# Optimization experiments

Hardware: AMD Instinct MI355X
Metric: run time of the kernel (lower is better)

The kernel has to match this reference:

```python
import jax, jax.numpy as jnp
import numpy as np

N_AGENTS = 64
B = 256
D = 256  # hidden_size == comm_dim


def setup_inputs() -> dict:
    key = jax.random.key(0)
    ks = jax.random.split(key, 4)
    s = 1.0 / np.sqrt(D)
    return {
        "hidden_state": jax.random.normal(ks[0], (B * N_AGENTS, D), jnp.float32),
        "W_act": jax.random.normal(ks[1], (D, D), jnp.float32) * s,
        "b_act": jnp.zeros((D,), jnp.float32),
        "W_sum": jax.random.normal(ks[2], (D, D), jnp.float32) * s,
        "b_sum": jnp.zeros((D,), jnp.float32),
        "W_head": jax.random.normal(ks[3], (D, D), jnp.float32) * s,
        "b_head": jnp.zeros((D,), jnp.float32),
    }


def reference(hidden_state, W_act, b_act, W_sum, b_sum, W_head, b_head):
    n = N_AGENTS
    # comm_act linear: (b*n, D)
    comm = hidden_state @ W_act.T + b_act
    b = comm.shape[0] // n
    comm = comm.reshape(b, n, D)
    # comm_mask = ones(n,n) - eye(n); agents all alive, comm_action_one=True
    mask = (jnp.ones((n, n), comm.dtype) - jnp.eye(n, dtype=comm.dtype))
    # original: expand to (b,n,n,D), mask, divide by (n-1), sum over dim=1 (sender i)
    # fused equivalent: out[b,j,d] = sum_i mask[i,j] * comm[b,i,d] / (n-1)
    agg = jnp.einsum('ij,bid->bjd', mask, comm) / (n - 1)
    x = agg.reshape(b * n, D) @ W_sum.T + b_sum      # comm_sum_head
    out = jax.nn.relu(x @ W_head.T + b_head)          # comm_head + active_fun
    return out
```

## Files before the change

### kernel.cpp

```cpp
#include <hip/hip_runtime.h>
#include <hip/hip_bf16.h>

#define DIM 256
#define NAGENT 64
#define NBATCH 256

typedef __bf16 bf16_t;
typedef bf16_t bf16x4 __attribute__((ext_vector_type(4)));
typedef bf16_t bf16x8 __attribute__((ext_vector_type(8)));
typedef float f32x4 __attribute__((ext_vector_type(4)));

__global__ __launch_bounds__(1024) void prep_kernel(
    const float* __restrict__ Wh, const float* __restrict__ Ws,
    const float* __restrict__ Wa, const float* __restrict__ ba,
    const float* __restrict__ bs, const float* __restrict__ bh,
    bf16_t* __restrict__ Wc, float* __restrict__ bcw) {
  const int b = blockIdx.x;
  const int t = threadIdx.x;
  const int jg = t & 63;
  const int kc = t >> 6;

  __shared__ float whl[DIM];
  __shared__ float t1l[DIM];
  __shared__ f32x4 part[16][64];
  __shared__ float red[256];

  if (t < DIM) whl[t] = Wh[b * DIM + t];
  __syncthreads();

  {
    f32x4 a = {0.f, 0.f, 0.f, 0.f};
#pragma unroll
    for (int ki = 0; ki < 16; ++ki) {
      const int k = kc * 16 + ki;
      const f32x4 w4 = *(const f32x4*)&Ws[k * DIM + jg * 4];
      a += whl[k] * w4;
    }
    part[kc][jg] = a;
  }
  __syncthreads();
  if (t < 64) {
    f32x4 s = part[0][t];
#pragma unroll
    for (int kc2 = 1; kc2 < 16; ++kc2) s += part[kc2][t];
    *(f32x4*)&t1l[t * 4] = s;
  }
  __syncthreads();

  {
    f32x4 a = {0.f, 0.f, 0.f, 0.f};
#pragma unroll
    for (int ki = 0; ki < 16; ++ki) {
      const int k = kc * 16 + ki;
      const f32x4 w4 = *(const f32x4*)&Wa[k * DIM + jg * 4];
      a += t1l[k] * w4;
    }
    if (t < 256) red[t] = t1l[t] * ba[t] + whl[t] * bs[t];
    part[kc][jg] = a;
  }
  __syncthreads();
  if (t < 64) {
    f32x4 s = part[0][t];
#pragma unroll
    for (int kc2 = 1; kc2 < 16; ++kc2) s += part[kc2][t];
    bf16x4 wb;
    wb[0] = (bf16_t)s[0]; wb[1] = (bf16_t)s[1];
    wb[2] = (bf16_t)s[2]; wb[3] = (bf16_t)s[3];
    *(bf16x4*)&Wc[b * DIM + t * 4] = wb;
    float p = red[t] + red[t + 64] + red[t + 128] + red[t + 192];
#pragma unroll
    for (int s2 = 32; s2 > 0; s2 >>= 1) p += __shfl_down(p, s2, 64);
    if (t == 0) bcw[b] = p + bh[b];
  }
}

__global__ __launch_bounds__(512) void fused_kernel(
    const float* __restrict__ h, const bf16_t* __restrict__ Wc,
    const float* __restrict__ bcw, float* __restrict__ out) {
  const int b = blockIdx.x;
  const int t = threadIdx.x;

  __shared__ __align__(16) bf16_t g[NAGENT * DIM];
  __shared__ f32x4 ps[8][64];

  const float* hb = h + (size_t)b * NAGENT * DIM;
  const int cg = t & 63;
  const int rg = t >> 6;

  f32x4 v[8];
  f32x4 s4 = {0.f, 0.f, 0.f, 0.f};
#pragma unroll
  for (int i = 0; i < 8; ++i) {
    v[i] = *(const f32x4*)&hb[(rg * 8 + i) * DIM + cg * 4];
    s4 += v[i];
  }
  ps[rg][cg] = s4;
  __syncthreads();
  f32x4 hs = ps[0][cg];
#pragma unroll
  for (int r = 1; r < 8; ++r) hs += ps[r][cg];

  const float inv = 1.0f / 63.0f;
#pragma unroll
  for (int i = 0; i < 8; ++i) {
    const int row = rg * 8 + i;
    const f32x4 gv = (hs - v[i]) * inv;
    bf16x4 gb;
    gb[0] = (bf16_t)gv[0]; gb[1] = (bf16_t)gv[1];
    gb[2] = (bf16_t)gv[2]; gb[3] = (bf16_t)gv[3];
    *(bf16x4*)&g[row * DIM + ((cg * 4) ^ ((row & 7) << 3))] = gb;
  }
  __syncthreads();

  const int w = t >> 6, lane = t & 63;
  const int lrow = lane & 15, lgrp = lane >> 4;

  f32x4 acc[4][2];
#pragma unroll
  for (int rt = 0; rt < 4; ++rt)
#pragma unroll
    for (int ct = 0; ct < 2; ++ct) acc[rt][ct] = (f32x4){0.f, 0.f, 0.f, 0.f};

#pragma unroll
  for (int kk = 0; kk < 8; ++kk) {
    const int k0 = kk * 32 + lgrp * 8;
    bf16x8 bfrag[2];
#pragma unroll
    for (int ct = 0; ct < 2; ++ct) {
      const int col = w * 32 + ct * 16 + lrow;
      bfrag[ct] = *(const bf16x8*)&Wc[col * DIM + k0];
    }
#pragma unroll
    for (int rt = 0; rt < 4; ++rt) {
      const int arow = rt * 16 + lrow;
      const bf16x8 afrag =
          *(const bf16x8*)&g[arow * DIM + (k0 ^ ((arow & 7) << 3))];
      acc[rt][0] = __builtin_amdgcn_mfma_f32_16x16x32_bf16(afrag, bfrag[0], acc[rt][0], 0, 0, 0);
      acc[rt][1] = __builtin_amdgcn_mfma_f32_16x16x32_bf16(afrag, bfrag[1], acc[rt][1], 0, 0, 0);
    }
  }

  float* ob = out + (size_t)b * NAGENT * DIM;
#pragma unroll
  for (int ct = 0; ct < 2; ++ct) {
    const int col = w * 32 + ct * 16 + lrow;
    const float bcv = bcw[col];
#pragma unroll
    for (int rt = 0; rt < 4; ++rt) {
#pragma unroll
      for (int r = 0; r < 4; ++r) {
        const int row = rt * 16 + lgrp * 4 + r;
        const float val = acc[rt][ct][r] + bcv;
        ob[row * DIM + col] = val > 0.f ? val : 0.f;
      }
    }
  }
}

extern "C" void kernel_launch(void* const* d_in, const int* in_sizes, int n_in,
                              void* d_out, int out_size, void* d_ws, size_t ws_size,
                              hipStream_t stream) {
  const float* h  = (const float*)d_in[0];
  const float* Wa = (const float*)d_in[1];
  const float* ba = (const float*)d_in[2];
  const float* Ws = (const float*)d_in[3];
  const float* bs = (const float*)d_in[4];
  const float* Wh = (const float*)d_in[5];
  const float* bh = (const float*)d_in[6];
  float* out = (float*)d_out;

  char* ws = (char*)d_ws;
  bf16_t* Wc  = (bf16_t*)ws;
  float*  bcw = (float*)(ws + 128 * 1024);

  prep_kernel<<<NBATCH, 1024, 0, stream>>>(Wh, Ws, Wa, ba, bs, bh, Wc, bcw);
  fused_kernel<<<NBATCH, 512, 0, stream>>>(h, Wc, bcw, out);
}
```

Baseline: 23.65 us.

## Fuse weight-prep and main kernels via grid-wide atomic readiness barrier

Merges the weight-composition prep kernel into the main fused kernel. Each block computes one row of the combined weight and bias, publishes it, and increments a global ready counter. It then overlaps the hidden-state load and aggregation with that work and spin-waits until all 256 blocks have finished before starting the MFMA GEMM. This removes a kernel launch and the inter-kernel gap, but adds a memset, a spin barrier that relies on all 256 blocks being co-resident, and 512-thread prep work in place of 1024 threads.

Result: slower. 67.83 us (+186.7%).

```diff
diff --git a/kernel.cpp b/kernel.cpp
--- a/kernel.cpp
+++ b/kernel.cpp
@@ -10,39 +10,45 @@
 typedef bf16_t bf16x8 __attribute__((ext_vector_type(8)));
 typedef float f32x4 __attribute__((ext_vector_type(4)));
 
-__global__ __launch_bounds__(1024) void prep_kernel(
+__global__ __launch_bounds__(512) void mac_one_kernel(
+    const float* __restrict__ h,
     const float* __restrict__ Wh, const float* __restrict__ Ws,
     const float* __restrict__ Wa, const float* __restrict__ ba,
     const float* __restrict__ bs, const float* __restrict__ bh,
-    bf16_t* __restrict__ Wc, float* __restrict__ bcw) {
+    bf16_t* __restrict__ Wc, float* __restrict__ bcw,
+    unsigned int* ready, float* __restrict__ out) {
   const int b = blockIdx.x;
   const int t = threadIdx.x;
-  const int jg = t & 63;
-  const int kc = t >> 6;
+  const int cg = t & 63;
+  const int rg = t >> 6;
 
-  __shared__ float whl[DIM];
+  __shared__ __align__(16) bf16_t g[NAGENT * DIM];
+  __shared__ f32x4 ps[8][64];
+  __shared__ f32x4 part[8][64];
   __shared__ float t1l[DIM];
-  __shared__ f32x4 part[16][64];
-  __shared__ float red[256];
 
-  if (t < DIM) whl[t] = Wh[b * DIM + t];
-  __syncthreads();
+  const float* hb = h + (size_t)b * NAGENT * DIM;
+
+  f32x4 v[8];
+#pragma unroll
+  for (int i = 0; i < 8; ++i)
+    v[i] = *(const f32x4*)&hb[(rg * 8 + i) * DIM + cg * 4];
 
   {
     f32x4 a = {0.f, 0.f, 0.f, 0.f};
 #pragma unroll
-    for (int ki = 0; ki < 16; ++ki) {
-      const int k = kc * 16 + ki;
-      const f32x4 w4 = *(const f32x4*)&Ws[k * DIM + jg * 4];
-      a += whl[k] * w4;
+    for (int ki = 0; ki < 32; ++ki) {
+      const int k = rg * 32 + ki;
+      const float wv = Wh[b * DIM + k];
+      a += wv * *(const f32x4*)&Ws[k * DIM + cg * 4];
     }
-    part[kc][jg] = a;
+    part[rg][cg] = a;
   }
   __syncthreads();
   if (t < 64) {
     f32x4 s = part[0][t];
 #pragma unroll
-    for (int kc2 = 1; kc2 < 16; ++kc2) s += part[kc2][t];
+    for (int r = 1; r < 8; ++r) s += part[r][t];
     *(f32x4*)&t1l[t * 4] = s;
   }
   __syncthreads();
@@ -50,56 +56,44 @@
   {
     f32x4 a = {0.f, 0.f, 0.f, 0.f};
 #pragma unroll
-    for (int ki = 0; ki < 16; ++ki) {
-      const int k = kc * 16 + ki;
-      const f32x4 w4 = *(const f32x4*)&Wa[k * DIM + jg * 4];
-      a += t1l[k] * w4;
+    for (int ki = 0; ki < 32; ++ki) {
+      const int k = rg * 32 + ki;
+      a += t1l[k] * *(const f32x4*)&Wa[k * DIM + cg * 4];
     }
-    if (t < 256) red[t] = t1l[t] * ba[t] + whl[t] * bs[t];
-    part[kc][jg] = a;
+    f32x4 s4 = v[0];
+#pragma unroll
+    for (int i = 1; i < 8; ++i) s4 += v[i];
+    ps[rg][cg] = s4;
+    part[rg][cg] = a;
   }
   __syncthreads();
+
   if (t < 64) {
     f32x4 s = part[0][t];
 #pragma unroll
-    for (int kc2 = 1; kc2 < 16; ++kc2) s += part[kc2][t];
+    for (int r = 1; r < 8; ++r) s += part[r][t];
     bf16x4 wb;
     wb[0] = (bf16_t)s[0]; wb[1] = (bf16_t)s[1];
     wb[2] = (bf16_t)s[2]; wb[3] = (bf16_t)s[3];
     *(bf16x4*)&Wc[b * DIM + t * 4] = wb;
-    float p = red[t] + red[t + 64] + red[t + 128] + red[t + 192];
+    const f32x4 t14 = *(const f32x4*)&t1l[t * 4];
+    const f32x4 ba4 = *(const f32x4*)&ba[t * 4];
+    const f32x4 wh4 = *(const f32x4*)&Wh[b * DIM + t * 4];
+    const f32x4 bs4 = *(const f32x4*)&bs[t * 4];
+    const f32x4 pp = t14 * ba4 + wh4 * bs4;
+    float p = pp[0] + pp[1] + pp[2] + pp[3];
 #pragma unroll
     for (int s2 = 32; s2 > 0; s2 >>= 1) p += __shfl_down(p, s2, 64);
-    if (t == 0) bcw[b] = p + bh[b];
+    if (t == 0) {
+      bcw[b] = p + bh[b];
+      __threadfence();
+      atomicAdd(ready, 1u);
+    }
   }
-}
 
-__global__ __launch_bounds__(512) void fused_kernel(
-    const float* __restrict__ h, const bf16_t* __restrict__ Wc,
-    const float* __restrict__ bcw, float* __restrict__ out) {
-  const int b = blockIdx.x;
-  const int t = threadIdx.x;
-
-  __shared__ __align__(16) bf16_t g[NAGENT * DIM];
-  __shared__ f32x4 ps[8][64];
-
-  const float* hb = h + (size_t)b * NAGENT * DIM;
-  const int cg = t & 63;
-  const int rg = t >> 6;
-
-  f32x4 v[8];
-  f32x4 s4 = {0.f, 0.f, 0.f, 0.f};
-#pragma unroll
-  for (int i = 0; i < 8; ++i) {
-    v[i] = *(const f32x4*)&hb[(rg * 8 + i) * DIM + cg * 4];
-    s4 += v[i];
-  }
-  ps[rg][cg] = s4;
-  __syncthreads();
   f32x4 hs = ps[0][cg];
 #pragma unroll
   for (int r = 1; r < 8; ++r) hs += ps[r][cg];
-
   const float inv = 1.0f / 63.0f;
 #pragma unroll
   for (int i = 0; i < 8; ++i) {
@@ -112,7 +106,15 @@
   }
   __syncthreads();
 
-  const int w = t >> 6, lane = t & 63;
+  if (t == 0) {
+    while (__hip_atomic_load(ready, __ATOMIC_ACQUIRE,
+                             __HIP_MEMORY_SCOPE_AGENT) < NBATCH)
+      __builtin_amdgcn_s_sleep(4);
+  }
+  __syncthreads();
+  __threadfence();
+
+  const int w = rg, lane = t & 63;
   const int lrow = lane & 15, lgrp = lane >> 4;
 
   f32x4 acc[4][2];
@@ -172,7 +174,10 @@
   char* ws = (char*)d_ws;
   bf16_t* Wc  = (bf16_t*)ws;
   float*  bcw = (float*)(ws + 128 * 1024);
+  unsigned int* ready = (unsigned int*)(ws + 132 * 1024);
 
-  prep_kernel<<<NBATCH, 1024, 0, stream>>>(Wh, Ws, Wa, ba, bs, bh, Wc, bcw);
-  fused_kernel<<<NBATCH, 512, 0, stream>>>(h, Wc, bcw, out);
+  hipMemsetAsync(ready, 0, sizeof(unsigned int), stream);
+
+  mac_one_kernel<<<NBATCH, 512, 0, stream>>>(h, Wh, Ws, Wa, ba, bs, bh,
+                                             Wc, bcw, ready, out);
 }
```

## Replace weight-product precompute with three chained in-block MFMA GEMMs

Applied to the files above, without the earlier changes.

Removes the prep kernel that folded W_head·W_sum·W_act into one combined bf16 weight and bias. The single fused kernel now runs three successive MFMA GEMM stages per batch block, ping-ponging bf16 activations between two shared-memory buffers and converting fp32 weights to bf16 on the fly. This saves a kernel launch and the serial prep work, but triples the MFMA work and weight traffic per block, doubles LDS use, and rounds intermediates to bf16 more often.

Measured after the change: 35.28 us. 49.2% more time.

```diff
diff --git a/kernel.cpp b/kernel.cpp
--- a/kernel.cpp
+++ b/kernel.cpp
@@ -10,82 +10,84 @@
 typedef bf16_t bf16x8 __attribute__((ext_vector_type(8)));
 typedef float f32x4 __attribute__((ext_vector_type(4)));
 
-__global__ __launch_bounds__(1024) void prep_kernel(
-    const float* __restrict__ Wh, const float* __restrict__ Ws,
-    const float* __restrict__ Wa, const float* __restrict__ ba,
-    const float* __restrict__ bs, const float* __restrict__ bh,
-    bf16_t* __restrict__ Wc, float* __restrict__ bcw) {
-  const int b = blockIdx.x;
-  const int t = threadIdx.x;
-  const int jg = t & 63;
-  const int kc = t >> 6;
+template <bool FINAL>
+__device__ __forceinline__ void gemm_stage(
+    const bf16_t* gin, const float* __restrict__ W,
+    const float* __restrict__ bias, bf16_t* gout,
+    float* __restrict__ gmem_out, int w, int lane) {
+  const int lrow = lane & 15, lgrp = lane >> 4;
 
-  __shared__ float whl[DIM];
-  __shared__ float t1l[DIM];
-  __shared__ f32x4 part[16][64];
-  __shared__ float red[256];
+  f32x4 acc[4][2];
+#pragma unroll
+  for (int rt = 0; rt < 4; ++rt)
+#pragma unroll
+    for (int ct = 0; ct < 2; ++ct) acc[rt][ct] = (f32x4){0.f, 0.f, 0.f, 0.f};
 
-  if (t < DIM) whl[t] = Wh[b * DIM + t];
-  __syncthreads();
+  float bv[2];
+#pragma unroll
+  for (int ct = 0; ct < 2; ++ct) bv[ct] = bias[w * 32 + ct * 16 + lrow];
 
-  {
-    f32x4 a = {0.f, 0.f, 0.f, 0.f};
 #pragma unroll
-    for (int ki = 0; ki < 16; ++ki) {
-      const int k = kc * 16 + ki;
-      const f32x4 w4 = *(const f32x4*)&Ws[k * DIM + jg * 4];
-      a += whl[k] * w4;
+  for (int kk = 0; kk < 8; ++kk) {
+    const int k0 = kk * 32 + lgrp * 8;
+    bf16x8 bfrag[2];
+#pragma unroll
+    for (int ct = 0; ct < 2; ++ct) {
+      const int col = w * 32 + ct * 16 + lrow;
+      const f32x4 w0 = *(const f32x4*)&W[col * DIM + k0];
+      const f32x4 w1 = *(const f32x4*)&W[col * DIM + k0 + 4];
+      bf16x8 bf;
+      bf[0] = (bf16_t)w0[0]; bf[1] = (bf16_t)w0[1];
+      bf[2] = (bf16_t)w0[2]; bf[3] = (bf16_t)w0[3];
+      bf[4] = (bf16_t)w1[0]; bf[5] = (bf16_t)w1[1];
+      bf[6] = (bf16_t)w1[2]; bf[7] = (bf16_t)w1[3];
+      bfrag[ct] = bf;
     }
-    part[kc][jg] = a;
+#pragma unroll
+    for (int rt = 0; rt < 4; ++rt) {
+      const int arow = rt * 16 + lrow;
+      const bf16x8 afrag =
+          *(const bf16x8*)&gin[arow * DIM + (k0 ^ ((arow & 7) << 3))];
+      acc[rt][0] = __builtin_amdgcn_mfma_f32_16x16x32_bf16(afrag, bfrag[0], acc[rt][0], 0, 0, 0);
+      acc[rt][1] = __builtin_amdgcn_mfma_f32_16x16x32_bf16(afrag, bfrag[1], acc[rt][1], 0, 0, 0);
+    }
   }
-  __syncthreads();
-  if (t < 64) {
-    f32x4 s = part[0][t];
+
 #pragma unroll
-    for (int kc2 = 1; kc2 < 16; ++kc2) s += part[kc2][t];
-    *(f32x4*)&t1l[t * 4] = s;
-  }
-  __syncthreads();
-
-  {
-    f32x4 a = {0.f, 0.f, 0.f, 0.f};
+  for (int ct = 0; ct < 2; ++ct) {
+    const int col = w * 32 + ct * 16 + lrow;
 #pragma unroll
-    for (int ki = 0; ki < 16; ++ki) {
-      const int k = kc * 16 + ki;
-      const f32x4 w4 = *(const f32x4*)&Wa[k * DIM + jg * 4];
-      a += t1l[k] * w4;
+    for (int rt = 0; rt < 4; ++rt) {
+#pragma unroll
+      for (int r = 0; r < 4; ++r) {
+        const int row = rt * 16 + lgrp * 4 + r;
+        float val = acc[rt][ct][r] + bv[ct];
+        if (FINAL) {
+          gmem_out[row * DIM + col] = val > 0.f ? val : 0.f;
+        } else {
+          gout[row * DIM + (col ^ ((row & 7) << 3))] = (bf16_t)val;
+        }
+      }
     }
-    if (t < 256) red[t] = t1l[t] * ba[t] + whl[t] * bs[t];
-    part[kc][jg] = a;
-  }
-  __syncthreads();
-  if (t < 64) {
-    f32x4 s = part[0][t];
-#pragma unroll
-    for (int kc2 = 1; kc2 < 16; ++kc2) s += part[kc2][t];
-    bf16x4 wb;
-    wb[0] = (bf16_t)s[0]; wb[1] = (bf16_t)s[1];
-    wb[2] = (bf16_t)s[2]; wb[3] = (bf16_t)s[3];
-    *(bf16x4*)&Wc[b * DIM + t * 4] = wb;
-    float p = red[t] + red[t + 64] + red[t + 128] + red[t + 192];
-#pragma unroll
-    for (int s2 = 32; s2 > 0; s2 >>= 1) p += __shfl_down(p, s2, 64);
-    if (t == 0) bcw[b] = p + bh[b];
   }
 }
 
-__global__ __launch_bounds__(512) void fused_kernel(
-    const float* __restrict__ h, const bf16_t* __restrict__ Wc,
-    const float* __restrict__ bcw, float* __restrict__ out) {
+__global__ __launch_bounds__(512) void mac3_kernel(
+    const float* __restrict__ h,
+    const float* __restrict__ Wa, const float* __restrict__ ba,
+    const float* __restrict__ Ws, const float* __restrict__ bs,
+    const float* __restrict__ Wh, const float* __restrict__ bh,
+    float* __restrict__ out) {
   const int b = blockIdx.x;
   const int t = threadIdx.x;
+  const int cg = t & 63;
+  const int rg = t >> 6;
 
-  __shared__ __align__(16) bf16_t g[NAGENT * DIM];
+  __shared__ __align__(16) bf16_t gA[NAGENT * DIM];
+  __shared__ __align__(16) bf16_t gB[NAGENT * DIM];
   __shared__ f32x4 ps[8][64];
 
   const float* hb = h + (size_t)b * NAGENT * DIM;
-  const int cg = t & 63;
-  const int rg = t >> 6;
 
   f32x4 v[8];
   f32x4 s4 = {0.f, 0.f, 0.f, 0.f};
@@ -108,53 +110,18 @@
     bf16x4 gb;
     gb[0] = (bf16_t)gv[0]; gb[1] = (bf16_t)gv[1];
     gb[2] = (bf16_t)gv[2]; gb[3] = (bf16_t)gv[3];
-    *(bf16x4*)&g[row * DIM + ((cg * 4) ^ ((row & 7) << 3))] = gb;
+    *(bf16x4*)&gA[row * DIM + ((cg * 4) ^ ((row & 7) << 3))] = gb;
   }
   __syncthreads();
 
-  const int w = t >> 6, lane = t & 63;
-  const int lrow = lane & 15, lgrp = lane >> 4;
+  const int w = rg, lane = t & 63;
+  float* ob = out + (size_t)b * NAGENT * DIM;
 
-  f32x4 acc[4][2];
-#pragma unroll
-  for (int rt = 0; rt < 4; ++rt)
-#pragma unroll
-    for (int ct = 0; ct < 2; ++ct) acc[rt][ct] = (f32x4){0.f, 0.f, 0.f, 0.f};
-
-#pragma unroll
-  for (int kk = 0; kk < 8; ++kk) {
-    const int k0 = kk * 32 + lgrp * 8;
-    bf16x8 bfrag[2];
-#pragma unroll
-    for (int ct = 0; ct < 2; ++ct) {
-      const int col = w * 32 + ct * 16 + lrow;
-      bfrag[ct] = *(const bf16x8*)&Wc[col * DIM + k0];
-    }
-#pragma unroll
-    for (int rt = 0; rt < 4; ++rt) {
-      const int arow = rt * 16 + lrow;
-      const bf16x8 afrag =
-          *(const bf16x8*)&g[arow * DIM + (k0 ^ ((arow & 7) << 3))];
-      acc[rt][0] = __builtin_amdgcn_mfma_f32_16x16x32_bf16(afrag, bfrag[0], acc[rt][0], 0, 0, 0);
-      acc[rt][1] = __builtin_amdgcn_mfma_f32_16x16x32_bf16(afrag, bfrag[1], acc[rt][1], 0, 0, 0);
-    }
-  }
-
-  float* ob = out + (size_t)b * NAGENT * DIM;
-#pragma unroll
-  for (int ct = 0; ct < 2; ++ct) {
-    const int col = w * 32 + ct * 16 + lrow;
-    const float bcv = bcw[col];
-#pragma unroll
-    for (int rt = 0; rt < 4; ++rt) {
-#pragma unroll
-      for (int r = 0; r < 4; ++r) {
-        const int row = rt * 16 + lgrp * 4 + r;
-        const float val = acc[rt][ct][r] + bcv;
-        ob[row * DIM + col] = val > 0.f ? val : 0.f;
-      }
-    }
-  }
+  gemm_stage<false>(gA, Wa, ba, gB, nullptr, w, lane);
+  __syncthreads();
+  gemm_stage<false>(gB, Ws, bs, gA, nullptr, w, lane);
+  __syncthreads();
+  gemm_stage<true>(gA, Wh, bh, nullptr, ob, w, lane);
 }
 
 extern "C" void kernel_launch(void* const* d_in, const int* in_sizes, int n_in,
@@ -169,10 +136,5 @@
   const float* bh = (const float*)d_in[6];
   float* out = (float*)d_out;
 
-  char* ws = (char*)d_ws;
-  bf16_t* Wc  = (bf16_t*)ws;
-  float*  bcw = (float*)(ws + 128 * 1024);
-
-  prep_kernel<<<NBATCH, 1024, 0, stream>>>(Wh, Ws, Wa, ba, bs, bh, Wc, bcw);
-  fused_kernel<<<NBATCH, 512, 0, stream>>>(h, Wc, bcw, out);
+  mac3_kernel<<<NBATCH, 512, 0, stream>>>(h, Wa, ba, Ws, bs, Wh, bh, out);
 }
```
